# Kernel optimization log

Measured on AMD Instinct MI355X. Metric: run time of the kernel, lower is better.

Reference implementation:

```python
import jax, jax.numpy as jnp
import numpy as np
import math

L, D_T, D, NL, NH, FFN, C, B = 24, 1024, 256, 12, 4, 1024, 2, 2048
HD = D // NH


def _layernorm(x, g, b, eps=1e-5):
    m = jnp.mean(x, axis=-1, keepdims=True)
    v = jnp.mean(jnp.square(x - m), axis=-1, keepdims=True)
    return (x - m) * jax.lax.rsqrt(v + eps) * g + b


def _rotate_half(x):
    x1, x2 = jnp.split(x, 2, axis=-1)
    return jnp.concatenate([-x2, x1], axis=-1)


def setup_inputs() -> dict:
    key = jax.random.key(0)
    ks = iter(jax.random.split(key, 64))
    n = lambda shape, s=0.02: jax.random.normal(next(ks), shape, dtype=jnp.float32) * s
    inp = {}
    inp['teacher_cls'] = jax.random.normal(next(ks), (B, L, D_T), dtype=jnp.float32)
    # input LN + projection
    inp['in_ln_g'] = jnp.ones((D_T,), jnp.float32); inp['in_ln_b'] = jnp.zeros((D_T,), jnp.float32)
    inp['proj_w'] = n((D, D_T)); inp['proj_b'] = jnp.zeros((D,), jnp.float32)
    # RoPE caches (buffers)
    inv_freq = 1.0 / (10000.0 ** (np.arange(0, D, 2, dtype=np.float32) / D))
    t = np.arange(L, dtype=np.float32)
    freqs = np.einsum('i,j->ij', t, inv_freq)
    emb = np.concatenate([freqs, freqs], axis=-1)
    inp['cos_cached'] = jnp.asarray(np.cos(emb)[None])  # [1,L,D]
    inp['sin_cached'] = jnp.asarray(np.sin(emb)[None])
    inp['pre_ln_g'] = jnp.ones((D,), jnp.float32); inp['pre_ln_b'] = jnp.zeros((D,), jnp.float32)
    # stacked transformer layer params [NL, ...]
    inp['l_ln1_g'] = jnp.ones((NL, D), jnp.float32); inp['l_ln1_b'] = jnp.zeros((NL, D), jnp.float32)
    inp['l_inw'] = n((NL, 3 * D, D)); inp['l_inb'] = jnp.zeros((NL, 3 * D), jnp.float32)
    inp['l_outw'] = n((NL, D, D)); inp['l_outb'] = jnp.zeros((NL, D), jnp.float32)
    inp['l_ln2_g'] = jnp.ones((NL, D), jnp.float32); inp['l_ln2_b'] = jnp.zeros((NL, D), jnp.float32)
    inp['l_w12'] = n((NL, 2 * FFN, D)); inp['l_b12'] = jnp.zeros((NL, 2 * FFN), jnp.float32)
    inp['l_w3'] = n((NL, D, FFN)); inp['l_b3'] = jnp.zeros((NL, D), jnp.float32)
    inp['post_ln_g'] = jnp.ones((D,), jnp.float32); inp['post_ln_b'] = jnp.zeros((D,), jnp.float32)
    # entropy gate
    inp['eg_w1'] = n((L, D, 8), 0.01); inp['eg_b1'] = jnp.zeros((L, 8), jnp.float32)
    inp['eg_w2'] = n((L, 8, 1), 0.01); inp['eg_b2'] = jnp.zeros((L, 1), jnp.float32)
    # per-position heads (stacked)
    inp['halt_w'] = n((L, D + 1)); inp['halt_b'] = jnp.full((L,), -4.0, jnp.float32)
    inp['cls_w'] = n((L, C, D)); inp['cls_b'] = jnp.zeros((L, C), jnp.float32)
    return inp


def _mha(x, inw, inb, outw, outb, mask):
    Bb, Ll, Dd = x.shape
    qkv = x @ inw.T + inb                              # [B,L,3D]
    q, k, v = jnp.split(qkv, 3, axis=-1)
    def heads(t):
        return t.reshape(Bb, Ll, NH, HD).transpose(0, 2, 1, 3)  # [B,H,L,hd]
    q, k, v = heads(q), heads(k), heads(v)
    scores = jnp.einsum('bhqd,bhkd->bhqk', q, k) / math.sqrt(HD)
    scores = jnp.where(mask, -jnp.inf, scores)
    attn = jax.nn.softmax(scores, axis=-1)
    o = jnp.einsum('bhqk,bhkd->bhqd', attn, v)
    o = o.transpose(0, 2, 1, 3).reshape(Bb, Ll, Dd)
    return o @ outw.T + outb


def reference(teacher_cls, in_ln_g, in_ln_b, proj_w, proj_b, cos_cached, sin_cached,
              pre_ln_g, pre_ln_b, l_ln1_g, l_ln1_b, l_inw, l_inb, l_outw, l_outb,
              l_ln2_g, l_ln2_b, l_w12, l_b12, l_w3, l_b3, post_ln_g, post_ln_b,
              eg_w1, eg_b1, eg_w2, eg_b2, halt_w, halt_b, cls_w, cls_b):
    x = _layernorm(teacher_cls, in_ln_g, in_ln_b)
    x = x @ proj_w.T + proj_b                          # [B,L,D]
    x = x * cos_cached + _rotate_half(x) * sin_cached  # RoPE
    z = _layernorm(x, pre_ln_g, pre_ln_b)
    mask = jnp.triu(jnp.ones((L, L), bool), 1)         # causal
    for i in range(NL):
        xn = _layernorm(z, l_ln1_g[i], l_ln1_b[i])
        z = z + _mha(xn, l_inw[i], l_inb[i], l_outw[i], l_outb[i], mask)
        xn = _layernorm(z, l_ln2_g[i], l_ln2_b[i])
        w12_out = xn @ l_w12[i].T + l_b12[i]           # [B,L,2*FFN]
        x1, x2 = jnp.split(w12_out, 2, axis=-1)
        hidden = jax.nn.silu(x1) * x2
        z = z + hidden @ l_w3[i].T + l_b3[i]
    z = _layernorm(z, post_ln_g, post_ln_b)
    # batched per-position classifier heads
    class_logits = jnp.einsum('bld,lcd->blc', z, cls_w) + cls_b   # [B,L,C]
    log_probs = jax.nn.log_softmax(class_logits, axis=-1)
    probs = jnp.exp(log_probs)
    probs_safe = jnp.clip(probs, 1e-10, 1.0)
    ent = -jnp.sum(probs_safe * jnp.log(probs_safe), axis=-1, keepdims=True)
    ent_norm = jnp.clip(ent / math.log(C), 0.0, 1.0)              # [B,L,1]
    # entropy gate
    h = jnp.tanh(jnp.einsum('bld,ldh->blh', z, eg_w1) + eg_b1)
    gate = jax.nn.sigmoid(jnp.einsum('blh,lho->blo', h, eg_w2) + eg_b2)
    gated = ent_norm * gate                                        # [B,L,1]
    # batched per-position halting heads
    combined = jnp.concatenate([z, gated], axis=-1)                # [B,L,D+1]
    halting_logits = jnp.einsum('bld,ld->bl', combined, halt_w) + halt_b
    return (halting_logits, class_logits, z)
```

## Files before the change

kernel.cpp:

```cpp
#include <hip/hip_runtime.h>
#include <hip/hip_bf16.h>
#include <math.h>

#define L_SEQ 24
#define DT 1024
#define DM 256
#define NLAYER 12
#define NHEAD 4
#define HDIM 64
#define FFND 1024
#define NCLS 2
#define NBATCH 2048
#define NTOK (NBATCH*L_SEQ)

typedef float f32x4 __attribute__((ext_vector_type(4)));
typedef __bf16 bf16x4 __attribute__((ext_vector_type(4)));
typedef __bf16 bf16x8 __attribute__((ext_vector_type(8)));

#define GLDS16(gp, lp) __builtin_amdgcn_global_load_lds((const __attribute__((address_space(1))) void*)(gp), (__attribute__((address_space(3))) void*)(lp), 16, 0, 0)

__device__ inline float wred_sum(float v){
#pragma unroll
  for (int o = 32; o > 0; o >>= 1) v += __shfl_xor(v, o);
  return v;
}
__device__ inline float wred_max(float v){
#pragma unroll
  for (int o = 32; o > 0; o >>= 1) v = fmaxf(v, __shfl_xor(v, o));
  return v;
}

__device__ __forceinline__ void stage16x32(const __bf16* __restrict__ g, int ldk, int k0,
                                           __bf16* ldsbase, int lane, int rowbase){
  int r = rowbase + (lane >> 2);
  int cs = (lane & 3) ^ ((lane >> 3) & 3);
  GLDS16(g + (size_t)r*ldk + k0 + cs*8, ldsbase);
}
__device__ __forceinline__ bf16x8 frag32(const __bf16* tile, int row, int lane){
  int p = (lane >> 4) ^ ((row >> 1) & 3);
  return *(const bf16x8*)(tile + (row << 5) + (p << 3));
}

__global__ void cvt_bf16_kernel(const float* __restrict__ in, __bf16* __restrict__ out, int n4){
  int i = blockIdx.x * blockDim.x + threadIdx.x;
  int stride = gridDim.x * blockDim.x;
  for (; i < n4; i += stride){
    float4 v = ((const float4*)in)[i];
    bf16x4 o;
    o[0] = (__bf16)v.x; o[1] = (__bf16)v.y; o[2] = (__bf16)v.z; o[3] = (__bf16)v.w;
    ((bf16x4*)out)[i] = o;
  }
}

__global__ __launch_bounds__(256) void ln1024_kernel(
    const float* __restrict__ in, const float* __restrict__ g, const float* __restrict__ bb,
    __bf16* __restrict__ out){
  int row = blockIdx.x;
  int tid = threadIdx.x, wid = tid >> 6, lane = tid & 63;
  float4 x = ((const float4*)(in + (size_t)row*DT))[tid];
  float s = x.x + x.y + x.z + x.w;
  float q = x.x*x.x + x.y*x.y + x.z*x.z + x.w*x.w;
  s = wred_sum(s); q = wred_sum(q);
  __shared__ float red[8];
  if (lane == 0){ red[wid] = s; red[4+wid] = q; }
  __syncthreads();
  s = red[0]+red[1]+red[2]+red[3];
  q = red[4]+red[5]+red[6]+red[7];
  float mean = s * (1.f/DT);
  float rstd = rsqrtf(q*(1.f/DT) - mean*mean + 1e-5f);
  float4 gv = ((const float4*)g)[tid], bv = ((const float4*)bb)[tid];
  bf16x4 o;
  o[0] = (__bf16)((x.x-mean)*rstd*gv.x + bv.x);
  o[1] = (__bf16)((x.y-mean)*rstd*gv.y + bv.y);
  o[2] = (__bf16)((x.z-mean)*rstd*gv.z + bv.z);
  o[3] = (__bf16)((x.w-mean)*rstd*gv.w + bv.w);
  ((bf16x4*)(out + (size_t)row*DT))[tid] = o;
}

__global__ __launch_bounds__(256) void rope_preln_kernel(
    float* __restrict__ z, const float* __restrict__ cosc, const float* __restrict__ sinc,
    const float* __restrict__ g, const float* __restrict__ bb,
    const float* __restrict__ g1, const float* __restrict__ b1, __bf16* __restrict__ xnb){
  int row = blockIdx.x*4 + (threadIdx.x >> 6);
  int lane = threadIdx.x & 63;
  int l = row % L_SEQ;
  float4 x = ((const float4*)(z + (size_t)row*DM))[lane];
  float4 p;
  p.x = __shfl_xor(x.x, 32); p.y = __shfl_xor(x.y, 32);
  p.z = __shfl_xor(x.z, 32); p.w = __shfl_xor(x.w, 32);
  float sgn = (lane < 32) ? -1.f : 1.f;
  float4 c = ((const float4*)(cosc + l*DM))[lane];
  float4 sn = ((const float4*)(sinc + l*DM))[lane];
  float4 xr;
  xr.x = x.x*c.x + sgn*p.x*sn.x;
  xr.y = x.y*c.y + sgn*p.y*sn.y;
  xr.z = x.z*c.z + sgn*p.z*sn.z;
  xr.w = x.w*c.w + sgn*p.w*sn.w;
  float s = wred_sum(xr.x + xr.y + xr.z + xr.w);
  float q = wred_sum(xr.x*xr.x + xr.y*xr.y + xr.z*xr.z + xr.w*xr.w);
  float mean = s * (1.f/DM);
  float rstd = rsqrtf(q*(1.f/DM) - mean*mean + 1e-5f);
  float4 gv = ((const float4*)g)[lane], bv = ((const float4*)bb)[lane];
  float4 y;
  y.x = (xr.x-mean)*rstd*gv.x + bv.x;
  y.y = (xr.y-mean)*rstd*gv.y + bv.y;
  y.z = (xr.z-mean)*rstd*gv.z + bv.z;
  y.w = (xr.w-mean)*rstd*gv.w + bv.w;
  ((float4*)(z + (size_t)row*DM))[lane] = y;
  float s2 = wred_sum(y.x + y.y + y.z + y.w);
  float q2 = wred_sum(y.x*y.x + y.y*y.y + y.z*y.z + y.w*y.w);
  float mean2 = s2 * (1.f/DM);
  float rstd2 = rsqrtf(q2*(1.f/DM) - mean2*mean2 + 1e-5f);
  float4 g1v = ((const float4*)g1)[lane], b1v = ((const float4*)b1)[lane];
  bf16x4 o;
  o[0] = (__bf16)((y.x-mean2)*rstd2*g1v.x + b1v.x);
  o[1] = (__bf16)((y.y-mean2)*rstd2*g1v.y + b1v.y);
  o[2] = (__bf16)((y.z-mean2)*rstd2*g1v.z + b1v.z);
  o[3] = (__bf16)((y.w-mean2)*rstd2*g1v.w + b1v.w);
  ((bf16x4*)(xnb + (size_t)row*DM))[lane] = o;
}

template<int MODE, int K>
__global__ __launch_bounds__(256) void gemm128_kernel(
    const __bf16* __restrict__ A, const __bf16* __restrict__ W,
    const float* __restrict__ bias,
    float* __restrict__ Cf, __bf16* __restrict__ Cb,
    int N, int nt){
  __shared__ __align__(16) __bf16 As[2][128*32];
  __shared__ __align__(16) __bf16 Bs[2][128*32];
  int bm = blockIdx.x / nt, bn = blockIdx.x % nt;
  int wid = threadIdx.x >> 6, lane = threadIdx.x & 63;
  int wr = wid >> 1, wc = wid & 1;
  int li = lane & 15, g4 = (lane >> 4) << 2;
  f32x4 acc[4][4] = {};
  const __bf16* ga = A + (size_t)bm*128*K;
  const __bf16* gb = W + (size_t)bn*128*K;
  const int NT = K/32;
  auto STAGE = [&](int b, int t){
    int k0 = t*32;
    stage16x32(ga, K, k0, &As[b][(wid*32)<<5],      lane, wid*32);
    stage16x32(ga, K, k0, &As[b][(wid*32+16)<<5],   lane, wid*32+16);
    stage16x32(gb, K, k0, &Bs[b][(wid*32)<<5],      lane, wid*32);
    stage16x32(gb, K, k0, &Bs[b][(wid*32+16)<<5],   lane, wid*32+16);
  };
  STAGE(0, 0);
  __syncthreads();
  int cur = 0;
  for (int t = 0; t < NT; t++){
    if (t + 1 < NT) STAGE(cur^1, t+1);
    bf16x8 xf[4], wf[4];
#pragma unroll
    for (int mi = 0; mi < 4; mi++) xf[mi] = frag32(As[cur], wr*64 + mi*16 + li, lane);
#pragma unroll
    for (int ni = 0; ni < 4; ni++) wf[ni] = frag32(Bs[cur], wc*64 + ni*16 + li, lane);
#pragma unroll
    for (int ni = 0; ni < 4; ni++)
#pragma unroll
      for (int mi = 0; mi < 4; mi++)
        acc[ni][mi] = __builtin_amdgcn_mfma_f32_16x16x32_bf16(wf[ni], xf[mi], acc[ni][mi], 0, 0, 0);
    __syncthreads();
    cur ^= 1;
  }
#pragma unroll
  for (int mi = 0; mi < 4; mi++){
    int m = bm*128 + wr*64 + mi*16 + li;
#pragma unroll
    for (int ni = 0; ni < 4; ni++){
      int n = bn*128 + wc*64 + ni*16 + g4;
      f32x4 bv = *(const f32x4*)(bias + n);
      f32x4 o = acc[ni][mi] + bv;
      if (MODE == 0){
        *(f32x4*)(Cf + (size_t)m*N + n) = o;
      } else {
        bf16x4 ob;
        ob[0] = (__bf16)o[0]; ob[1] = (__bf16)o[1]; ob[2] = (__bf16)o[2]; ob[3] = (__bf16)o[3];
        *(bf16x4*)(Cb + (size_t)m*N + n) = ob;
      }
    }
  }
}

__global__ __launch_bounds__(256) void gemm_glu_kernel(
    const __bf16* __restrict__ A, const __bf16* __restrict__ W12,
    const float* __restrict__ bias, __bf16* __restrict__ H){
  __shared__ __align__(16) __bf16 As[2][128*32];
  __shared__ __align__(16) __bf16 B1s[2][128*32];
  __shared__ __align__(16) __bf16 B2s[2][128*32];
  const int K = 256;
  int bm = blockIdx.x >> 3, bn = blockIdx.x & 7;
  int wid = threadIdx.x >> 6, lane = threadIdx.x & 63;
  int wr = wid >> 1, wc = wid & 1;
  int li = lane & 15, g4 = (lane >> 4) << 2;
  f32x4 acc1[4][4] = {}, acc2[4][4] = {};
  const __bf16* ga  = A   + (size_t)bm*128*K;
  const __bf16* gb1 = W12 + (size_t)bn*128*K;
  const __bf16* gb2 = gb1 + (size_t)1024*K;
  auto STAGE = [&](int b, int t){
    int k0 = t*32;
    stage16x32(ga,  K, k0, &As[b][(wid*32)<<5],     lane, wid*32);
    stage16x32(ga,  K, k0, &As[b][(wid*32+16)<<5],  lane, wid*32+16);
    stage16x32(gb1, K, k0, &B1s[b][(wid*32)<<5],    lane, wid*32);
    stage16x32(gb1, K, k0, &B1s[b][(wid*32+16)<<5], lane, wid*32+16);
    stage16x32(gb2, K, k0, &B2s[b][(wid*32)<<5],    lane, wid*32);
    stage16x32(gb2, K, k0, &B2s[b][(wid*32+16)<<5], lane, wid*32+16);
  };
  STAGE(0, 0);
  __syncthreads();
  int cur = 0;
  for (int t = 0; t < 8; t++){
    if (t < 7) STAGE(cur^1, t+1);
    bf16x8 xf[4], w1f[4], w2f[4];
#pragma unroll
    for (int mi = 0; mi < 4; mi++) xf[mi] = frag32(As[cur], wr*64 + mi*16 + li, lane);
#pragma unroll
    for (int ni = 0; ni < 4; ni++){
      w1f[ni] = frag32(B1s[cur], wc*64 + ni*16 + li, lane);
      w2f[ni] = frag32(B2s[cur], wc*64 + ni*16 + li, lane);
    }
#pragma unroll
    for (int ni = 0; ni < 4; ni++)
#pragma unroll
      for (int mi = 0; mi < 4; mi++){
        acc1[ni][mi] = __builtin_amdgcn_mfma_f32_16x16x32_bf16(w1f[ni], xf[mi], acc1[ni][mi], 0, 0, 0);
        acc2[ni][mi] = __builtin_amdgcn_mfma_f32_16x16x32_bf16(w2f[ni], xf[mi], acc2[ni][mi], 0, 0, 0);
      }
    __syncthreads();
    cur ^= 1;
  }
#pragma unroll
  for (int mi = 0; mi < 4; mi++){
    int m = bm*128 + wr*64 + mi*16 + li;
#pragma unroll
    for (int ni = 0; ni < 4; ni++){
      int n = bn*128 + wc*64 + ni*16 + g4;
      f32x4 b1v = *(const f32x4*)(bias + n);
      f32x4 b2v = *(const f32x4*)(bias + 1024 + n);
      bf16x4 ob;
#pragma unroll
      for (int r = 0; r < 4; r++){
        float v1 = acc1[ni][mi][r] + b1v[r];
        float v2 = acc2[ni][mi][r] + b2v[r];
        float sig = 1.f/(1.f + __expf(-v1));
        ob[r] = (__bf16)(v1*sig*v2);
      }
      *(bf16x4*)(H + (size_t)m*FFND + n) = ob;
    }
  }
}

template<int K>
__global__ __launch_bounds__(256) void gemm_ln_kernel(
    const __bf16* __restrict__ A, const __bf16* __restrict__ W,
    const float* __restrict__ bias, float* __restrict__ z,
    const float* __restrict__ lng, const float* __restrict__ lnb,
    __bf16* __restrict__ outb, float* __restrict__ outf){
  __shared__ __align__(16) __bf16 As[2][64*32];
  __shared__ __align__(16) __bf16 Bs[2][256*32];
  __shared__ float redS[64][4], redQ[64][4];
  int bm = blockIdx.x;
  int wid = threadIdx.x >> 6, lane = threadIdx.x & 63;
  int li = lane & 15, g4 = (lane >> 4) << 2;
  f32x4 acc[4][4] = {};
  const __bf16* ga = A + (size_t)bm*64*K;
  const int NT = K/32;
  auto STAGE = [&](int b, int t){
    int k0 = t*32;
    stage16x32(ga, K, k0, &As[b][(wid*16)<<5], lane, wid*16);
#pragma unroll
    for (int j = 0; j < 4; j++)
      stage16x32(W, K, k0, &Bs[b][(wid*64 + j*16)<<5], lane, wid*64 + j*16);
  };
  STAGE(0, 0);
  __syncthreads();
  int cur = 0;
  for (int t = 0; t < NT; t++){
    if (t + 1 < NT) STAGE(cur^1, t+1);
    bf16x8 xf[4], wf[4];
#pragma unroll
    for (int mi = 0; mi < 4; mi++) xf[mi] = frag32(As[cur], mi*16 + li, lane);
#pragma unroll
    for (int ni = 0; ni < 4; ni++) wf[ni] = frag32(Bs[cur], wid*64 + ni*16 + li, lane);
#pragma unroll
    for (int ni = 0; ni < 4; ni++)
#pragma unroll
      for (int mi = 0; mi < 4; mi++)
        acc[ni][mi] = __builtin_amdgcn_mfma_f32_16x16x32_bf16(wf[ni], xf[mi], acc[ni][mi], 0, 0, 0);
    __syncthreads();
    cur ^= 1;
  }
  float sA[4] = {}, qA[4] = {};
#pragma unroll
  for (int mi = 0; mi < 4; mi++){
    int m = bm*64 + mi*16 + li;
#pragma unroll
    for (int ni = 0; ni < 4; ni++){
      int n = wid*64 + ni*16 + g4;
      f32x4 zv = *(const f32x4*)(z + (size_t)m*DM + n);
      f32x4 bv = *(const f32x4*)(bias + n);
      f32x4 v = acc[ni][mi] + bv + zv;
      acc[ni][mi] = v;
      *(f32x4*)(z + (size_t)m*DM + n) = v;
#pragma unroll
      for (int r = 0; r < 4; r++){ sA[mi] += v[r]; qA[mi] += v[r]*v[r]; }
    }
  }
#pragma unroll
  for (int mi = 0; mi < 4; mi++){
    float s = sA[mi], q = qA[mi];
    s += __shfl_xor(s, 16); q += __shfl_xor(q, 16);
    s += __shfl_xor(s, 32); q += __shfl_xor(q, 32);
    if ((lane >> 4) == 0){ redS[mi*16 + li][wid] = s; redQ[mi*16 + li][wid] = q; }
  }
  __syncthreads();
#pragma unroll
  for (int mi = 0; mi < 4; mi++){
    int ml = mi*16 + li;
    float s = redS[ml][0] + redS[ml][1] + redS[ml][2] + redS[ml][3];
    float q = redQ[ml][0] + redQ[ml][1] + redQ[ml][2] + redQ[ml][3];
    float mean = s * (1.f/DM);
    float rstd = rsqrtf(q*(1.f/DM) - mean*mean + 1e-5f);
    int m = bm*64 + ml;
#pragma unroll
    for (int ni = 0; ni < 4; ni++){
      int n = wid*64 + ni*16 + g4;
      f32x4 gv = *(const f32x4*)(lng + n);
      f32x4 bv = *(const f32x4*)(lnb + n);
      if (outb){
        bf16x4 o;
#pragma unroll
        for (int r = 0; r < 4; r++) o[r] = (__bf16)((acc[ni][mi][r] - mean)*rstd*gv[r] + bv[r]);
        *(bf16x4*)(outb + (size_t)m*DM + n) = o;
      } else {
        f32x4 o;
#pragma unroll
        for (int r = 0; r < 4; r++) o[r] = (acc[ni][mi][r] - mean)*rstd*gv[r] + bv[r];
        *(f32x4*)(outf + (size_t)m*DM + n) = o;
      }
    }
  }
}

__global__ __launch_bounds__(256) void attn_kernel(const __bf16* __restrict__ qkv, __bf16* __restrict__ ob){
  int b = blockIdx.x;
  int h = threadIdx.x >> 6, lane = threadIdx.x & 63;
  __shared__ __align__(16) __bf16 Qs[NHEAD][L_SEQ][HDIM];
  __shared__ __align__(16) __bf16 Ks[NHEAD][L_SEQ][HDIM];
  __shared__ float Ps[NHEAD][L_SEQ][L_SEQ];
  const __bf16* base = qkv + (size_t)b*L_SEQ*768;
  float V[L_SEQ];
#pragma unroll
  for (int t = 0; t < L_SEQ; t++){
    int sw = lane ^ ((t & 7) << 3);
    Qs[h][t][sw] = base[t*768 + h*64 + lane];
    Ks[h][t][sw] = base[t*768 + 256 + h*64 + lane];
    V[t] = (float)base[t*768 + 512 + h*64 + lane];
  }
  __syncthreads();
  for (int p = lane; p < L_SEQ*L_SEQ; p += 64){
    int q = p / L_SEQ, k = p - q*L_SEQ;
    if (k <= q){
      int qx = (q & 7) << 3, kx = (k & 7) << 3;
      const __bf16* qr = Qs[h][q];
      const __bf16* kr = Ks[h][k];
      float s = 0.f;
#pragma unroll
      for (int d = 0; d < 64; d += 4){
        bf16x4 qa = *(const bf16x4*)(qr + (d ^ qx));
        bf16x4 ka = *(const bf16x4*)(kr + (d ^ kx));
        s += (float)qa[0]*(float)ka[0] + (float)qa[1]*(float)ka[1]
           + (float)qa[2]*(float)ka[2] + (float)qa[3]*(float)ka[3];
      }
      Ps[h][q][k] = s * 0.125f;
    }
  }
  __syncthreads();
  for (int q = 0; q < L_SEQ; q++){
    float v = (lane <= q) ? Ps[h][q][lane] : -1e30f;
    float mx = wred_max(v);
    float e = (lane <= q) ? __expf(v - mx) : 0.f;
    float sm = wred_sum(e);
    if (lane < L_SEQ) Ps[h][q][lane] = e / sm;
  }
  __syncthreads();
  for (int q = 0; q < L_SEQ; q++){
    float o = 0.f;
    for (int k = 0; k <= q; k++) o += Ps[h][q][k] * V[k];
    ob[((size_t)b*L_SEQ + q)*DM + h*64 + lane] = (__bf16)o;
  }
}

__global__ __launch_bounds__(256) void heads_kernel(
    const float* __restrict__ z,
    const float* __restrict__ cls_w, const float* __restrict__ cls_b,
    const float* __restrict__ eg_w1, const float* __restrict__ eg_b1,
    const float* __restrict__ eg_w2, const float* __restrict__ eg_b2,
    const float* __restrict__ halt_w, const float* __restrict__ halt_b,
    float* __restrict__ halt_out, float* __restrict__ cls_out){
  int m = blockIdx.x*4 + (threadIdx.x >> 6);
  int lane = threadIdx.x & 63;
  int l = m % L_SEQ;
  float4 zv = ((const float4*)(z + (size_t)m*DM))[lane];
  float4 w0 = ((const float4*)(cls_w + ((size_t)l*2 + 0)*DM))[lane];
  float4 w1 = ((const float4*)(cls_w + ((size_t)l*2 + 1)*DM))[lane];
  float c0 = wred_sum(zv.x*w0.x + zv.y*w0.y + zv.z*w0.z + zv.w*w0.w) + cls_b[l*2 + 0];
  float c1 = wred_sum(zv.x*w1.x + zv.y*w1.y + zv.z*w1.z + zv.w*w1.w) + cls_b[l*2 + 1];
  float mx = fmaxf(c0, c1);
  float e0 = __expf(c0 - mx), e1 = __expf(c1 - mx);
  float inv = 1.f/(e0 + e1);
  float p0 = fminf(fmaxf(e0*inv, 1e-10f), 1.f);
  float p1 = fminf(fmaxf(e1*inv, 1e-10f), 1.f);
  float ent = -(p0*__logf(p0) + p1*__logf(p1));
  float entn = fminf(fmaxf(ent * 1.44269504f, 0.f), 1.f);
  const float4* wg = (const float4*)(eg_w1 + ((size_t)l*DM + 4*lane)*8);
  float hacc[8] = {};
#pragma unroll
  for (int dd = 0; dd < 4; dd++){
    float zd = (dd==0) ? zv.x : (dd==1) ? zv.y : (dd==2) ? zv.z : zv.w;
    float4 a = wg[dd*2], b = wg[dd*2 + 1];
    hacc[0] += zd*a.x; hacc[1] += zd*a.y; hacc[2] += zd*a.z; hacc[3] += zd*a.w;
    hacc[4] += zd*b.x; hacc[5] += zd*b.y; hacc[6] += zd*b.z; hacc[7] += zd*b.w;
  }
  float gin = 0.f;
#pragma unroll
  for (int j = 0; j < 8; j++){
    float hj = wred_sum(hacc[j]);
    hj = tanhf(hj + eg_b1[l*8 + j]);
    gin += hj * eg_w2[l*8 + j];
  }
  gin += eg_b2[l];
  float gate = 1.f/(1.f + __expf(-gin));
  float gated = entn * gate;
  const float* hw = halt_w + (size_t)l*257;
  float hp = zv.x*hw[4*lane] + zv.y*hw[4*lane+1] + zv.z*hw[4*lane+2] + zv.w*hw[4*lane+3];
  float hl = wred_sum(hp) + gated*hw[256] + halt_b[l];
  if (lane == 0) halt_out[m] = hl;
  if (lane < 2) cls_out[(size_t)m*2 + lane] = lane ? c1 : c0;
}

extern "C" void kernel_launch(void* const* d_in, const int* in_sizes, int n_in,
                              void* d_out, int out_size, void* d_ws, size_t ws_size,
                              hipStream_t stream){
  const float* teacher = (const float*)d_in[0];
  const float* in_ln_g = (const float*)d_in[1];
  const float* in_ln_b = (const float*)d_in[2];
  const float* proj_w  = (const float*)d_in[3];
  const float* proj_b  = (const float*)d_in[4];
  const float* cosc    = (const float*)d_in[5];
  const float* sinc    = (const float*)d_in[6];
  const float* pre_g   = (const float*)d_in[7];
  const float* pre_b   = (const float*)d_in[8];
  const float* l_ln1_g = (const float*)d_in[9];
  const float* l_ln1_b = (const float*)d_in[10];
  const float* l_inw   = (const float*)d_in[11];
  const float* l_inb   = (const float*)d_in[12];
  const float* l_outw  = (const float*)d_in[13];
  const float* l_outb  = (const float*)d_in[14];
  const float* l_ln2_g = (const float*)d_in[15];
  const float* l_ln2_b = (const float*)d_in[16];
  const float* l_w12   = (const float*)d_in[17];
  const float* l_b12   = (const float*)d_in[18];
  const float* l_w3    = (const float*)d_in[19];
  const float* l_b3    = (const float*)d_in[20];
  const float* post_g  = (const float*)d_in[21];
  const float* post_b  = (const float*)d_in[22];
  const float* eg_w1   = (const float*)d_in[23];
  const float* eg_b1   = (const float*)d_in[24];
  const float* eg_w2   = (const float*)d_in[25];
  const float* eg_b2   = (const float*)d_in[26];
  const float* halt_w  = (const float*)d_in[27];
  const float* halt_b  = (const float*)d_in[28];
  const float* cls_w   = (const float*)d_in[29];
  const float* cls_b   = (const float*)d_in[30];

  float* out = (float*)d_out;
  float* halt_out = out;
  float* cls_out  = out + NTOK;
  float* z_out    = out + NTOK + (size_t)NTOK*NCLS;

  char* ws = (char*)d_ws;
  size_t off = 0;
  auto alloc = [&](size_t bytes){ void* p = ws + off; off += (bytes + 255) & ~(size_t)255; return p; };
  float*  zbuf = (float*) alloc((size_t)NTOK*DM*4);
  __bf16* xnb  = (__bf16*)alloc((size_t)NTOK*DM*2);
  __bf16* qkvb = (__bf16*)alloc((size_t)NTOK*768*2);
  __bf16* obuf = (__bf16*)alloc((size_t)NTOK*DM*2);
  __bf16* bigb = (__bf16*)alloc((size_t)NTOK*1024*2);
  __bf16* w_proj = (__bf16*)alloc((size_t)262144*2);
  __bf16* w_in   = (__bf16*)alloc((size_t)2359296*2);
  __bf16* w_out  = (__bf16*)alloc((size_t)786432*2);
  __bf16* w_12   = (__bf16*)alloc((size_t)6291456*2);
  __bf16* w_3    = (__bf16*)alloc((size_t)3145728*2);

  cvt_bf16_kernel<<<256, 256, 0, stream>>>(proj_w, w_proj, 262144/4);
  cvt_bf16_kernel<<<1024, 256, 0, stream>>>(l_inw, w_in, 2359296/4);
  cvt_bf16_kernel<<<512, 256, 0, stream>>>(l_outw, w_out, 786432/4);
  cvt_bf16_kernel<<<2048, 256, 0, stream>>>(l_w12, w_12, 6291456/4);
  cvt_bf16_kernel<<<1024, 256, 0, stream>>>(l_w3, w_3, 3145728/4);

  ln1024_kernel<<<NTOK, 256, 0, stream>>>(teacher, in_ln_g, in_ln_b, bigb);
  gemm128_kernel<0, 1024><<<384*2, 256, 0, stream>>>(bigb, w_proj, proj_b, zbuf, nullptr, 256, 2);
  rope_preln_kernel<<<NTOK/4, 256, 0, stream>>>(zbuf, cosc, sinc, pre_g, pre_b, l_ln1_g, l_ln1_b, xnb);

  for (int i = 0; i < NLAYER; i++){
    gemm128_kernel<1, 256><<<384*6, 256, 0, stream>>>(xnb, w_in + (size_t)i*768*256, l_inb + i*768, nullptr, qkvb, 768, 6);
    attn_kernel<<<NBATCH, 256, 0, stream>>>(qkvb, obuf);
    gemm_ln_kernel<256><<<NTOK/64, 256, 0, stream>>>(obuf, w_out + (size_t)i*256*256, l_outb + i*256,
                                                     zbuf, l_ln2_g + i*256, l_ln2_b + i*256, xnb, nullptr);
    gemm_glu_kernel<<<384*8, 256, 0, stream>>>(xnb, w_12 + (size_t)i*2048*256, l_b12 + i*2048, bigb);
    bool last = (i == NLAYER-1);
    gemm_ln_kernel<1024><<<NTOK/64, 256, 0, stream>>>(bigb, w_3 + (size_t)i*256*1024, l_b3 + i*256,
                                                      zbuf,
                                                      last ? post_g : l_ln1_g + (i+1)*256,
                                                      last ? post_b : l_ln1_b + (i+1)*256,
                                                      last ? nullptr : xnb,
                                                      last ? z_out : nullptr);
  }

  heads_kernel<<<NTOK/4, 256, 0, stream>>>(z_out, cls_w, cls_b, eg_w1, eg_b1, eg_w2, eg_b2,
                                           halt_w, halt_b, halt_out, cls_out);
}
```

Measured before the change: 4.517 ms.

## Deepen GEMM prefetch to two stages with explicit waitcnt and XCD-aware block remap

The three bf16 GEMM kernels now issue LDS prefetches two k-tiles ahead. Each iteration waits with explicit vmcnt counts plus raw s_barrier instead of a full __syncthreads, so global loads overlap the MFMA work better. Block indices are remapped so consecutive tiles land on the same XCD for better L2 reuse, and MFMA sections get raised wave priority. The risk is fragile hand-counted waitcnt values that must match the number of loads issued per stage, and a barrier was added before the LN reduction to keep it correct.

New measurement: 4.093 ms. -9.4%, faster.

```diff
diff --git a/kernel.cpp b/kernel.cpp
--- a/kernel.cpp
+++ b/kernel.cpp
@@ -18,6 +18,8 @@
 typedef __bf16 bf16x8 __attribute__((ext_vector_type(8)));
 
 #define GLDS16(gp, lp) __builtin_amdgcn_global_load_lds((const __attribute__((address_space(1))) void*)(gp), (__attribute__((address_space(3))) void*)(lp), 16, 0, 0)
+#define VMWAIT(N) asm volatile("s_waitcnt vmcnt(" #N ")" ::: "memory")
+#define LGKM0()   asm volatile("s_waitcnt lgkmcnt(0)" ::: "memory")
 
 __device__ inline float wred_sum(float v){
 #pragma unroll
@@ -39,6 +41,11 @@
 __device__ __forceinline__ bf16x8 frag32(const __bf16* tile, int row, int lane){
   int p = (lane >> 4) ^ ((row >> 1) & 3);
   return *(const bf16x8*)(tile + (row << 5) + (p << 3));
+}
+
+__device__ __forceinline__ int xcd_work(){
+  int nwg = gridDim.x, bid = blockIdx.x;
+  return (bid & 7) * (nwg >> 3) + (bid >> 3);
 }
 
 __global__ void cvt_bf16_kernel(const float* __restrict__ in, __bf16* __restrict__ out, int n4){
@@ -128,7 +135,8 @@
     int N, int nt){
   __shared__ __align__(16) __bf16 As[2][128*32];
   __shared__ __align__(16) __bf16 Bs[2][128*32];
-  int bm = blockIdx.x / nt, bn = blockIdx.x % nt;
+  int work = xcd_work();
+  int bm = work / nt, bn = work % nt;
   int wid = threadIdx.x >> 6, lane = threadIdx.x & 63;
   int wr = wid >> 1, wc = wid & 1;
   int li = lane & 15, g4 = (lane >> 4) << 2;
@@ -144,21 +152,27 @@
     stage16x32(gb, K, k0, &Bs[b][(wid*32+16)<<5],   lane, wid*32+16);
   };
   STAGE(0, 0);
-  __syncthreads();
+  STAGE(1, 1);
   int cur = 0;
   for (int t = 0; t < NT; t++){
-    if (t + 1 < NT) STAGE(cur^1, t+1);
+    if (t + 1 < NT) { VMWAIT(4); } else { VMWAIT(0); }
+    __builtin_amdgcn_s_barrier();
     bf16x8 xf[4], wf[4];
 #pragma unroll
     for (int mi = 0; mi < 4; mi++) xf[mi] = frag32(As[cur], wr*64 + mi*16 + li, lane);
 #pragma unroll
     for (int ni = 0; ni < 4; ni++) wf[ni] = frag32(Bs[cur], wc*64 + ni*16 + li, lane);
+    LGKM0();
+    __builtin_amdgcn_sched_barrier(0);
+    __builtin_amdgcn_s_barrier();
+    if (t + 2 < NT) STAGE(cur, t+2);
+    __builtin_amdgcn_s_setprio(1);
 #pragma unroll
     for (int ni = 0; ni < 4; ni++)
 #pragma unroll
       for (int mi = 0; mi < 4; mi++)
         acc[ni][mi] = __builtin_amdgcn_mfma_f32_16x16x32_bf16(wf[ni], xf[mi], acc[ni][mi], 0, 0, 0);
-    __syncthreads();
+    __builtin_amdgcn_s_setprio(0);
     cur ^= 1;
   }
 #pragma unroll
@@ -187,7 +201,8 @@
   __shared__ __align__(16) __bf16 B1s[2][128*32];
   __shared__ __align__(16) __bf16 B2s[2][128*32];
   const int K = 256;
-  int bm = blockIdx.x >> 3, bn = blockIdx.x & 7;
+  int work = xcd_work();
+  int bm = work >> 3, bn = work & 7;
   int wid = threadIdx.x >> 6, lane = threadIdx.x & 63;
   int wr = wid >> 1, wc = wid & 1;
   int li = lane & 15, g4 = (lane >> 4) << 2;
@@ -205,10 +220,11 @@
     stage16x32(gb2, K, k0, &B2s[b][(wid*32+16)<<5], lane, wid*32+16);
   };
   STAGE(0, 0);
-  __syncthreads();
+  STAGE(1, 1);
   int cur = 0;
   for (int t = 0; t < 8; t++){
-    if (t < 7) STAGE(cur^1, t+1);
+    if (t + 1 < 8) { VMWAIT(6); } else { VMWAIT(0); }
+    __builtin_amdgcn_s_barrier();
     bf16x8 xf[4], w1f[4], w2f[4];
 #pragma unroll
     for (int mi = 0; mi < 4; mi++) xf[mi] = frag32(As[cur], wr*64 + mi*16 + li, lane);
@@ -217,6 +233,11 @@
       w1f[ni] = frag32(B1s[cur], wc*64 + ni*16 + li, lane);
       w2f[ni] = frag32(B2s[cur], wc*64 + ni*16 + li, lane);
     }
+    LGKM0();
+    __builtin_amdgcn_sched_barrier(0);
+    __builtin_amdgcn_s_barrier();
+    if (t + 2 < 8) STAGE(cur, t+2);
+    __builtin_amdgcn_s_setprio(1);
 #pragma unroll
     for (int ni = 0; ni < 4; ni++)
 #pragma unroll
@@ -224,7 +245,7 @@
         acc1[ni][mi] = __builtin_amdgcn_mfma_f32_16x16x32_bf16(w1f[ni], xf[mi], acc1[ni][mi], 0, 0, 0);
         acc2[ni][mi] = __builtin_amdgcn_mfma_f32_16x16x32_bf16(w2f[ni], xf[mi], acc2[ni][mi], 0, 0, 0);
       }
-    __syncthreads();
+    __builtin_amdgcn_s_setprio(0);
     cur ^= 1;
   }
 #pragma unroll
@@ -271,21 +292,27 @@
       stage16x32(W, K, k0, &Bs[b][(wid*64 + j*16)<<5], lane, wid*64 + j*16);
   };
   STAGE(0, 0);
-  __syncthreads();
+  STAGE(1, 1);
   int cur = 0;
   for (int t = 0; t < NT; t++){
-    if (t + 1 < NT) STAGE(cur^1, t+1);
+    if (t + 1 < NT) { VMWAIT(5); } else { VMWAIT(0); }
+    __builtin_amdgcn_s_barrier();
     bf16x8 xf[4], wf[4];
 #pragma unroll
     for (int mi = 0; mi < 4; mi++) xf[mi] = frag32(As[cur], mi*16 + li, lane);
 #pragma unroll
     for (int ni = 0; ni < 4; ni++) wf[ni] = frag32(Bs[cur], wid*64 + ni*16 + li, lane);
+    LGKM0();
+    __builtin_amdgcn_sched_barrier(0);
+    __builtin_amdgcn_s_barrier();
+    if (t + 2 < NT) STAGE(cur, t+2);
+    __builtin_amdgcn_s_setprio(1);
 #pragma unroll
     for (int ni = 0; ni < 4; ni++)
 #pragma unroll
       for (int mi = 0; mi < 4; mi++)
         acc[ni][mi] = __builtin_amdgcn_mfma_f32_16x16x32_bf16(wf[ni], xf[mi], acc[ni][mi], 0, 0, 0);
-    __syncthreads();
+    __builtin_amdgcn_s_setprio(0);
     cur ^= 1;
   }
   float sA[4] = {}, qA[4] = {};
@@ -304,6 +331,7 @@
       for (int r = 0; r < 4; r++){ sA[mi] += v[r]; qA[mi] += v[r]*v[r]; }
     }
   }
+  __syncthreads();
 #pragma unroll
   for (int mi = 0; mi < 4; mi++){
     float s = sA[mi], q = qA[mi];
```
